# Kernel tuning notes

Hardware: AMD Instinct MI355X
Metric: run time of the kernel (lower is better)

The kernel has to match this reference:

```python
import jax, jax.numpy as jnp
import numpy as np

B, N, C, C_OUT, E = 8, 1024, 256, 256, 16384


def setup_inputs() -> dict:
    key = jax.random.key(0)
    k1, k2, k3 = jax.random.split(key, 3)
    x = jax.random.normal(k1, (B, N, C), dtype=jnp.float32)
    edge_index = jax.random.randint(k2, (2, E, B), 0, N)  # [2, E, B], values in [0, N)
    W = jax.random.normal(k3, (C_OUT, C), dtype=jnp.float32) * 0.02  # torch Linear weight [out, in]
    b = jnp.zeros((C_OUT,), dtype=jnp.float32)
    return {"x": x, "edge_index": edge_index, "W": W, "b": b}


def reference(x, edge_index, W, b):
    Bs, Nn, Cc = x.shape
    BN = Bs * Nn
    # Vectorized version of the per-batch python loop: offset each graph's
    # node indices into the big block-diagonal adjacency.
    offs = jnp.arange(Bs, dtype=edge_index.dtype) * Nn          # [B]
    src = (edge_index[0] + offs[None, :]).reshape(-1)           # [E*B]
    dst = (edge_index[1] + offs[None, :]).reshape(-1)           # [E*B]
    adj = jnp.zeros((BN, BN), dtype=x.dtype).at[src, dst].set(1.0)
    adj = adj + jnp.eye(BN, dtype=x.dtype)                      # self loops (adds on top, as in torch code)
    D = adj.sum(axis=1)                                         # [BN]
    d_inv_sqrt = jnp.where(D > 0, jax.lax.rsqrt(D), 0.0)        # pow(-0.5) with inf -> 0
    adj_n = d_inv_sqrt[:, None] * adj * d_inv_sqrt[None, :]     # D^-1/2 A D^-1/2
    h = adj_n @ x.reshape(BN, Cc)                               # [BN, C]
    out = h @ W.T + b                                           # Linear
    return out.reshape(Bs, Nn, -1)
```

## Files before the change

kernel.cpp:

```cpp
#include <hip/hip_runtime.h>
#include <stdint.h>

#define B_   8
#define N_   1024
#define C_   256
#define E_   16384
#define BN_  (B_ * N_)
#define NW_  (N_ / 32)
#define NBR_CAP 64

typedef __attribute__((ext_vector_type(8))) short bf16x8;
typedef __attribute__((ext_vector_type(4))) float f32x4;

static __device__ __forceinline__ short f32_to_bf16(float f) {
  uint32_t u = __float_as_uint(f);
  uint32_t r = (u + 0x7fffu + ((u >> 16) & 1u)) >> 16;
  return (short)r;
}
static __device__ __forceinline__ float bf16_to_f32(short s) {
  return __uint_as_float(((uint32_t)(uint16_t)s) << 16);
}

__global__ __launch_bounds__(256) void scatter_edges(
    const int* __restrict__ ei, uint32_t* __restrict__ mask) {
  int t = blockIdx.x * 256 + threadIdx.x;
  if (t >= E_ * B_) return;
  int b   = t & (B_ - 1);
  int src = ei[t];
  int dst = ei[E_ * B_ + t];
  int row = b * N_ + src;
  atomicOr(&mask[row * NW_ + (dst >> 5)], 1u << (dst & 31));
}

__global__ __launch_bounds__(256) void degrees_nbr(
    const uint32_t* __restrict__ mask, float* __restrict__ dinv,
    int* __restrict__ deg, uint16_t* __restrict__ nbr) {
  int i = blockIdx.x * 256 + threadIdx.x;
  if (i >= BN_) return;
  const uint32_t* m = mask + i * NW_;
  uint16_t* row = nbr + i * NBR_CAP;
  int d = 0;
#pragma unroll
  for (int w = 0; w < NW_; w++) {
    uint32_t bits = m[w];
    while (bits) {
      int j = __ffs(bits) - 1;
      bits &= bits - 1;
      row[d++] = (uint16_t)(w * 32 + j);
    }
  }
  deg[i] = d;
  int dd = d;
  while (dd & 3) row[dd++] = 0;
  dinv[i] = rsqrtf((float)(d + 1));
}

__global__ __launch_bounds__(256) void gemm_bf16x3(
    const float* __restrict__ X, const float* __restrict__ W,
    const float* __restrict__ dinv, float* __restrict__ Z) {
  __shared__ __attribute__((aligned(16))) short Ah[64][40];
  __shared__ __attribute__((aligned(16))) short Al[64][40];
  __shared__ __attribute__((aligned(16))) short Bh[64][40];
  __shared__ __attribute__((aligned(16))) short Bl[64][40];

  int t  = threadIdx.x;
  int m0 = blockIdx.x * 64;
  int n0 = blockIdx.y * 64;
  int lr = t >> 2;
  int lc = (t & 3) * 8;
  int wv = t >> 6;
  int ln = t & 63;
  int lm = ln & 15;
  int qd = ln >> 4;

  f32x4 acc[4];
#pragma unroll
  for (int i = 0; i < 4; i++) acc[i] = (f32x4){0.f, 0.f, 0.f, 0.f};

  for (int k0 = 0; k0 < C_; k0 += 32) {
    const float* xr = &X[(size_t)(m0 + lr) * C_ + k0 + lc];
    const float* wr = &W[(size_t)(n0 + lr) * C_ + k0 + lc];
    float xv[8], wv8[8];
    *(float4*)&xv[0] = *(const float4*)&xr[0];
    *(float4*)&xv[4] = *(const float4*)&xr[4];
    *(float4*)&wv8[0] = *(const float4*)&wr[0];
    *(float4*)&wv8[4] = *(const float4*)&wr[4];
    bf16x8 xh, xl, wh, wl;
#pragma unroll
    for (int j = 0; j < 8; j++) {
      short h = f32_to_bf16(xv[j]);
      xh[j] = h;
      xl[j] = f32_to_bf16(xv[j] - bf16_to_f32(h));
      short g = f32_to_bf16(wv8[j]);
      wh[j] = g;
      wl[j] = f32_to_bf16(wv8[j] - bf16_to_f32(g));
    }
    *(bf16x8*)&Ah[lr][lc] = xh;
    *(bf16x8*)&Al[lr][lc] = xl;
    *(bf16x8*)&Bh[lr][lc] = wh;
    *(bf16x8*)&Bl[lr][lc] = wl;
    __syncthreads();

    bf16x8 ah = *(const bf16x8*)&Ah[16 * wv + lm][qd * 8];
    bf16x8 al = *(const bf16x8*)&Al[16 * wv + lm][qd * 8];
#pragma unroll
    for (int nt = 0; nt < 4; nt++) {
      bf16x8 bh = *(const bf16x8*)&Bh[nt * 16 + lm][qd * 8];
      bf16x8 bl = *(const bf16x8*)&Bl[nt * 16 + lm][qd * 8];
      acc[nt] = __builtin_amdgcn_mfma_f32_16x16x32_bf16(ah, bh, acc[nt], 0, 0, 0);
      acc[nt] = __builtin_amdgcn_mfma_f32_16x16x32_bf16(ah, bl, acc[nt], 0, 0, 0);
      acc[nt] = __builtin_amdgcn_mfma_f32_16x16x32_bf16(al, bh, acc[nt], 0, 0, 0);
    }
    __syncthreads();
  }

  float di[4];
#pragma unroll
  for (int r = 0; r < 4; r++) di[r] = dinv[m0 + 16 * wv + qd * 4 + r];
#pragma unroll
  for (int nt = 0; nt < 4; nt++) {
#pragma unroll
    for (int r = 0; r < 4; r++) {
      int m = m0 + 16 * wv + qd * 4 + r;
      int n = n0 + nt * 16 + lm;
      Z[(size_t)m * C_ + n] = di[r] * acc[nt][r];
    }
  }
}

__global__ __launch_bounds__(256) void aggregate(
    const uint16_t* __restrict__ nbr, const int* __restrict__ deg,
    const float* __restrict__ dinv, const float* __restrict__ Z,
    const float* __restrict__ bias, float* __restrict__ out) {
  int blk   = blockIdx.x;
  int batch = blk & 7;
  int group = blk >> 3;
  int wv    = threadIdx.x >> 6;
  int ln    = threadIdx.x & 63;
  int loc   = group * 4 + wv;
  int node  = batch * N_ + loc;
  int c4    = ln * 4;

  const float* zb = Z + (size_t)batch * N_ * C_;
  float4 acc = *(const float4*)&zb[(size_t)loc * C_ + c4];

  int d = deg[node];
  const uint16_t* nb = nbr + (size_t)node * NBR_CAP;
  for (int k = 0; k < d; k += 4) {
    ushort4 n4 = *(const ushort4*)&nb[k];
    float4 z0 = *(const float4*)&zb[(size_t)n4.x * C_ + c4];
    float4 z1 = *(const float4*)&zb[(size_t)n4.y * C_ + c4];
    float4 z2 = *(const float4*)&zb[(size_t)n4.z * C_ + c4];
    float4 z3 = *(const float4*)&zb[(size_t)n4.w * C_ + c4];
    float w1 = (k + 1 < d) ? 1.f : 0.f;
    float w2 = (k + 2 < d) ? 1.f : 0.f;
    float w3 = (k + 3 < d) ? 1.f : 0.f;
    acc.x += z0.x; acc.y += z0.y; acc.z += z0.z; acc.w += z0.w;
    acc.x += w1 * z1.x; acc.y += w1 * z1.y; acc.z += w1 * z1.z; acc.w += w1 * z1.w;
    acc.x += w2 * z2.x; acc.y += w2 * z2.y; acc.z += w2 * z2.z; acc.w += w2 * z2.w;
    acc.x += w3 * z3.x; acc.y += w3 * z3.y; acc.z += w3 * z3.z; acc.w += w3 * z3.w;
  }

  float di = dinv[node];
  float4 bb = *(const float4*)&bias[c4];
  float4 o;
  o.x = di * acc.x + bb.x;
  o.y = di * acc.y + bb.y;
  o.z = di * acc.z + bb.z;
  o.w = di * acc.w + bb.w;
  *(float4*)&out[(size_t)node * C_ + c4] = o;
}

extern "C" void kernel_launch(void* const* d_in, const int* in_sizes, int n_in,
                              void* d_out, int out_size, void* d_ws,
                              size_t ws_size, hipStream_t stream) {
  const float* x    = (const float*)d_in[0];
  const int*   ei   = (const int*)d_in[1];
  const float* W    = (const float*)d_in[2];
  const float* bias = (const float*)d_in[3];
  float*       out  = (float*)d_out;

  char* ws = (char*)d_ws;
  uint32_t* mask = (uint32_t*)(ws + 0x000000);
  float*    dinv = (float*)   (ws + 0x100000);
  int*      deg  = (int*)     (ws + 0x110000);
  uint16_t* nbr  = (uint16_t*)(ws + 0x120000);
  float*    Z    = (float*)   (ws + 0x220000);

  hipMemsetAsync(mask, 0, (size_t)BN_ * NW_ * 4, stream);

  scatter_edges<<<(E_ * B_) / 256, 256, 0, stream>>>(ei, mask);
  degrees_nbr<<<BN_ / 256, 256, 0, stream>>>(mask, dinv, deg, nbr);
  gemm_bf16x3<<<dim3(BN_ / 64, C_ / 64), 256, 0, stream>>>(x, W, dinv, Z);
  aggregate<<<BN_ / 4, 256, 0, stream>>>(nbr, deg, dinv, Z, bias, out);
}
```

Before: 106.5 us.

## Fuse degree and neighbor-list construction into GEMM and aggregate kernels

Removes the separate degrees_nbr kernel. The GEMM now computes row degrees with popcount over the bitmask and keeps dinv in shared memory. The aggregate kernel builds each node's neighbor list in LDS through a wave-wide prefix scan over the mask words. This saves one launch plus the global nbr, deg and dinv traffic, in exchange for recomputing degrees in every GEMM column block and a serial bit-extraction step per wave. The GEMM barrier placement also moves: the barrier now comes before the LDS stores instead of after the MFMAs.

```diff
diff --git a/kernel.cpp b/kernel.cpp
--- a/kernel.cpp
+++ b/kernel.cpp
@@ -7,7 +7,7 @@
 #define E_   16384
 #define BN_  (B_ * N_)
 #define NW_  (N_ / 32)
-#define NBR_CAP 64
+#define LIST_CAP 96
 
 typedef __attribute__((ext_vector_type(8))) short bf16x8;
 typedef __attribute__((ext_vector_type(4))) float f32x4;
@@ -32,40 +32,34 @@
   atomicOr(&mask[row * NW_ + (dst >> 5)], 1u << (dst & 31));
 }
 
-__global__ __launch_bounds__(256) void degrees_nbr(
-    const uint32_t* __restrict__ mask, float* __restrict__ dinv,
-    int* __restrict__ deg, uint16_t* __restrict__ nbr) {
-  int i = blockIdx.x * 256 + threadIdx.x;
-  if (i >= BN_) return;
-  const uint32_t* m = mask + i * NW_;
-  uint16_t* row = nbr + i * NBR_CAP;
-  int d = 0;
-#pragma unroll
-  for (int w = 0; w < NW_; w++) {
-    uint32_t bits = m[w];
-    while (bits) {
-      int j = __ffs(bits) - 1;
-      bits &= bits - 1;
-      row[d++] = (uint16_t)(w * 32 + j);
-    }
-  }
-  deg[i] = d;
-  int dd = d;
-  while (dd & 3) row[dd++] = 0;
-  dinv[i] = rsqrtf((float)(d + 1));
-}
-
 __global__ __launch_bounds__(256) void gemm_bf16x3(
     const float* __restrict__ X, const float* __restrict__ W,
-    const float* __restrict__ dinv, float* __restrict__ Z) {
+    const uint32_t* __restrict__ mask, float* __restrict__ Z) {
   __shared__ __attribute__((aligned(16))) short Ah[64][40];
   __shared__ __attribute__((aligned(16))) short Al[64][40];
   __shared__ __attribute__((aligned(16))) short Bh[64][40];
   __shared__ __attribute__((aligned(16))) short Bl[64][40];
+  __shared__ int   dpart[4][64];
+  __shared__ float dinv_s[64];
 
   int t  = threadIdx.x;
   int m0 = blockIdx.x * 64;
   int n0 = blockIdx.y * 64;
+
+  {
+    int row = t & 63, part = t >> 6;
+    const uint4* mp =
+        (const uint4*)&mask[(size_t)(m0 + row) * NW_ + part * 8];
+    uint4 a = mp[0], b = mp[1];
+    dpart[part][row] = __popc(a.x) + __popc(a.y) + __popc(a.z) + __popc(a.w) +
+                       __popc(b.x) + __popc(b.y) + __popc(b.z) + __popc(b.w);
+  }
+  __syncthreads();
+  if (t < 64) {
+    int d = dpart[0][t] + dpart[1][t] + dpart[2][t] + dpart[3][t] + 1;
+    dinv_s[t] = rsqrtf((float)d);
+  }
+
   int lr = t >> 2;
   int lc = (t & 3) * 8;
   int wv = t >> 6;
@@ -95,6 +89,7 @@
       wh[j] = g;
       wl[j] = f32_to_bf16(wv8[j] - bf16_to_f32(g));
     }
+    __syncthreads();
     *(bf16x8*)&Ah[lr][lc] = xh;
     *(bf16x8*)&Al[lr][lc] = xl;
     *(bf16x8*)&Bh[lr][lc] = wh;
@@ -111,12 +106,12 @@
       acc[nt] = __builtin_amdgcn_mfma_f32_16x16x32_bf16(ah, bl, acc[nt], 0, 0, 0);
       acc[nt] = __builtin_amdgcn_mfma_f32_16x16x32_bf16(al, bh, acc[nt], 0, 0, 0);
     }
-    __syncthreads();
-  }
+  }
+  __syncthreads();
 
   float di[4];
 #pragma unroll
-  for (int r = 0; r < 4; r++) di[r] = dinv[m0 + 16 * wv + qd * 4 + r];
+  for (int r = 0; r < 4; r++) di[r] = dinv_s[16 * wv + qd * 4 + r];
 #pragma unroll
   for (int nt = 0; nt < 4; nt++) {
 #pragma unroll
@@ -129,9 +124,10 @@
 }
 
 __global__ __launch_bounds__(256) void aggregate(
-    const uint16_t* __restrict__ nbr, const int* __restrict__ deg,
-    const float* __restrict__ dinv, const float* __restrict__ Z,
+    const uint32_t* __restrict__ mask, const float* __restrict__ Z,
     const float* __restrict__ bias, float* __restrict__ out) {
+  __shared__ uint16_t lists[4][LIST_CAP];
+
   int blk   = blockIdx.x;
   int batch = blk & 7;
   int group = blk >> 3;
@@ -141,34 +137,54 @@
   int node  = batch * N_ + loc;
   int c4    = ln * 4;
 
+  uint32_t bits = (ln < NW_) ? mask[(size_t)node * NW_ + ln] : 0u;
+  int cnt = __popc(bits);
+  int pfx = cnt;
+#pragma unroll
+  for (int off = 1; off < 64; off <<= 1) {
+    int v = __shfl_up(pfx, off);
+    if (ln >= off) pfx += v;
+  }
+  int total = __shfl(pfx, 63);
+  pfx -= cnt;
+  uint16_t* lst = lists[wv];
+  int o = pfx, jb = ln * 32;
+  while (bits) {
+    int j = __ffs(bits) - 1;
+    bits &= bits - 1;
+    lst[o++] = (uint16_t)(jb + j);
+  }
+  if (ln == 0) {
+    int dd = total;
+    while (dd & 3) lst[dd++] = 0;
+  }
+
   const float* zb = Z + (size_t)batch * N_ * C_;
   float4 acc = *(const float4*)&zb[(size_t)loc * C_ + c4];
 
-  int d = deg[node];
-  const uint16_t* nb = nbr + (size_t)node * NBR_CAP;
-  for (int k = 0; k < d; k += 4) {
-    ushort4 n4 = *(const ushort4*)&nb[k];
+  for (int k = 0; k < total; k += 4) {
+    ushort4 n4 = *(const ushort4*)&lst[k];
     float4 z0 = *(const float4*)&zb[(size_t)n4.x * C_ + c4];
     float4 z1 = *(const float4*)&zb[(size_t)n4.y * C_ + c4];
     float4 z2 = *(const float4*)&zb[(size_t)n4.z * C_ + c4];
     float4 z3 = *(const float4*)&zb[(size_t)n4.w * C_ + c4];
-    float w1 = (k + 1 < d) ? 1.f : 0.f;
-    float w2 = (k + 2 < d) ? 1.f : 0.f;
-    float w3 = (k + 3 < d) ? 1.f : 0.f;
+    float w1 = (k + 1 < total) ? 1.f : 0.f;
+    float w2 = (k + 2 < total) ? 1.f : 0.f;
+    float w3 = (k + 3 < total) ? 1.f : 0.f;
     acc.x += z0.x; acc.y += z0.y; acc.z += z0.z; acc.w += z0.w;
     acc.x += w1 * z1.x; acc.y += w1 * z1.y; acc.z += w1 * z1.z; acc.w += w1 * z1.w;
     acc.x += w2 * z2.x; acc.y += w2 * z2.y; acc.z += w2 * z2.z; acc.w += w2 * z2.w;
     acc.x += w3 * z3.x; acc.y += w3 * z3.y; acc.z += w3 * z3.z; acc.w += w3 * z3.w;
   }
 
-  float di = dinv[node];
+  float di = rsqrtf((float)(total + 1));
   float4 bb = *(const float4*)&bias[c4];
-  float4 o;
-  o.x = di * acc.x + bb.x;
-  o.y = di * acc.y + bb.y;
-  o.z = di * acc.z + bb.z;
-  o.w = di * acc.w + bb.w;
-  *(float4*)&out[(size_t)node * C_ + c4] = o;
+  float4 o4;
+  o4.x = di * acc.x + bb.x;
+  o4.y = di * acc.y + bb.y;
+  o4.z = di * acc.z + bb.z;
+  o4.w = di * acc.w + bb.w;
+  *(float4*)&out[(size_t)node * C_ + c4] = o4;
 }
 
 extern "C" void kernel_launch(void* const* d_in, const int* in_sizes, int n_in,
@@ -182,15 +198,11 @@
 
   char* ws = (char*)d_ws;
   uint32_t* mask = (uint32_t*)(ws + 0x000000);
-  float*    dinv = (float*)   (ws + 0x100000);
-  int*      deg  = (int*)     (ws + 0x110000);
-  uint16_t* nbr  = (uint16_t*)(ws + 0x120000);
-  float*    Z    = (float*)   (ws + 0x220000);
+  float*    Z    = (float*)   (ws + 0x100000);
 
   hipMemsetAsync(mask, 0, (size_t)BN_ * NW_ * 4, stream);
 
   scatter_edges<<<(E_ * B_) / 256, 256, 0, stream>>>(ei, mask);
-  degrees_nbr<<<BN_ / 256, 256, 0, stream>>>(mask, dinv, deg, nbr);
-  gemm_bf16x3<<<dim3(BN_ / 64, C_ / 64), 256, 0, stream>>>(x, W, dinv, Z);
-  aggregate<<<BN_ / 4, 256, 0, stream>>>(nbr, deg, dinv, Z, bias, out);
-}
+  gemm_bf16x3<<<dim3(BN_ / 64, C_ / 64), 256, 0, stream>>>(x, W, mask, Z);
+  aggregate<<<BN_ / 4, 256, 0, stream>>>(mask, Z, bias, out);
+}
```

Result: faster. 96.32 us (median of 2 runs) (-9.6%).
